# Optimization experiments

Measured on AMD Instinct MI355X. Metric: run time of the kernel, lower is better.

The kernel has to match this reference:

```python
import jax, jax.numpy as jnp
import numpy as np

B, L, D, H = 4, 2048, 1024, 64  # batch, seq, d_model, head_size

def setup_inputs() -> dict:
    key = jax.random.key(0)
    k1, k2 = jax.random.split(key)
    x = jax.random.normal(k1, (B, L, D), dtype=jnp.float32)
    # nn.Linear(d_model, head_size, bias=False) weight: [head_size, d_model]
    Wq = jax.random.normal(k2, (H, D), dtype=jnp.float32) * (1.0 / np.sqrt(D))
    return {"x": x, "Wq": Wq}

def reference(x, Wq):
    # Faithful to source bug: q, k, v ALL use the query projection.
    q = jnp.einsum('bld,hd->blh', x, Wq)
    k = q
    v = q
    d_k = x.shape[-1]  # source uses d_model, not head_size
    scores = jnp.einsum('blh,bmh->blm', q, k) / jnp.sqrt(jnp.float32(d_k))
    Lq = x.shape[1]
    causal = jnp.tril(jnp.ones((Lq, Lq), dtype=bool))
    scores = jnp.where(causal, scores, -jnp.inf)
    attn = jax.nn.softmax(scores, axis=-1)
    # dropout in eval mode -> identity
    return jnp.einsum('blm,bmh->blh', attn, v)
```

## Files before the change

### kernel.cpp

```cpp
#include <hip/hip_runtime.h>
#include <cmath>

#define Bb 4
#define Ll 2048
#define Dd 1024
#define Hh 64

#define QSCL 0.21233050f

typedef float f32x4 __attribute__((ext_vector_type(4)));
typedef short s16x8 __attribute__((ext_vector_type(8)));

__device__ __forceinline__ unsigned int cvtpk(float a, float b) {
    unsigned int r;
    asm("v_cvt_pk_bf16_f32 %0, %1, %2" : "=v"(r) : "v"(a), "v"(b));
    return r;
}

__device__ __forceinline__ void gload16(const void* g, void* l) {
    __builtin_amdgcn_global_load_lds((__attribute__((address_space(1))) const void*)g,
                                     (__attribute__((address_space(3))) void*)l, 16, 0, 0);
}

__global__ __launch_bounds__(256, 2) void proj_mfma(const float* __restrict__ x,
                                                    const float* __restrict__ Wq,
                                                    unsigned short* __restrict__ q,
                                                    unsigned short* __restrict__ qT) {
    __shared__ uint4 xs4[2][32 * 16];
    __shared__ uint4 ws4[2][32 * 64];
    const int t = threadIdx.x;
    const int lane = t & 63, w = t >> 6;
    const int m15 = lane & 15, q_ = lane >> 4;
    const int row0 = blockIdx.x * 16;
    const int kc = t & 31, rr = t >> 5;
    const float* xsrc0 = x + (size_t)(row0 + rr) * Dd + kc * 8;
    const float* xsrc1 = x + (size_t)(row0 + rr + 8) * Dd + kc * 8;

    float4 xa0 = *(const float4*)xsrc0, xb0 = *(const float4*)(xsrc0 + 4);
    float4 xa1 = *(const float4*)xsrc1, xb1 = *(const float4*)(xsrc1 + 4);
#pragma unroll
    for (int j = 0; j < 8; ++j) {
        int idx2 = t + j * 256;
        int kcw = idx2 & 31, hw = (idx2 >> 5) & 63;
        const float* wsrc = Wq + (size_t)hw * Dd + kcw * 8;
        float4 a = *(const float4*)wsrc;
        float4 b2 = *(const float4*)(wsrc + 4);
        uint4 p; p.x = cvtpk(a.x, a.y); p.y = cvtpk(a.z, a.w);
        p.z = cvtpk(b2.x, b2.y); p.w = cvtpk(b2.z, b2.w);
        ws4[0][kcw * 64 + (hw ^ kcw)] = p;
    }
    {
        uint4 p0; p0.x = cvtpk(xa0.x, xa0.y); p0.y = cvtpk(xa0.z, xa0.w);
        p0.z = cvtpk(xb0.x, xb0.y); p0.w = cvtpk(xb0.z, xb0.w);
        xs4[0][kc * 16 + (rr ^ (kc & 15))] = p0;
        uint4 p1; p1.x = cvtpk(xa1.x, xa1.y); p1.y = cvtpk(xa1.z, xa1.w);
        p1.z = cvtpk(xb1.x, xb1.y); p1.w = cvtpk(xb1.z, xb1.w);
        xs4[0][kc * 16 + ((rr + 8) ^ (kc & 15))] = p1;
    }
    xa0 = *(const float4*)(xsrc0 + 256); xb0 = *(const float4*)(xsrc0 + 260);
    xa1 = *(const float4*)(xsrc1 + 256); xb1 = *(const float4*)(xsrc1 + 260);

    f32x4 acc = {0.f, 0.f, 0.f, 0.f};
    for (int c = 0; c < 4; ++c) {
        const int p = c & 1;
        __syncthreads();
        if (c + 1 < 4) {
            const int k0n = (c + 1) * 256;
#pragma unroll
            for (int j = 0; j < 8; ++j) {
                int idx2 = t + j * 256;
                int kcw = idx2 & 31, hw = (idx2 >> 5) & 63;
                const float* wsrc = Wq + (size_t)hw * Dd + k0n + kcw * 8;
                float4 a = *(const float4*)wsrc;
                float4 b2 = *(const float4*)(wsrc + 4);
                uint4 pw; pw.x = cvtpk(a.x, a.y); pw.y = cvtpk(a.z, a.w);
                pw.z = cvtpk(b2.x, b2.y); pw.w = cvtpk(b2.z, b2.w);
                ws4[p ^ 1][kcw * 64 + (hw ^ kcw)] = pw;
            }
            uint4 p0; p0.x = cvtpk(xa0.x, xa0.y); p0.y = cvtpk(xa0.z, xa0.w);
            p0.z = cvtpk(xb0.x, xb0.y); p0.w = cvtpk(xb0.z, xb0.w);
            xs4[p ^ 1][kc * 16 + (rr ^ (kc & 15))] = p0;
            uint4 p1; p1.x = cvtpk(xa1.x, xa1.y); p1.y = cvtpk(xa1.z, xa1.w);
            p1.z = cvtpk(xb1.x, xb1.y); p1.w = cvtpk(xb1.z, xb1.w);
            xs4[p ^ 1][kc * 16 + ((rr + 8) ^ (kc & 15))] = p1;
            if (c + 2 < 4) {
                xa0 = *(const float4*)(xsrc0 + (c + 2) * 256);
                xb0 = *(const float4*)(xsrc0 + (c + 2) * 256 + 4);
                xa1 = *(const float4*)(xsrc1 + (c + 2) * 256);
                xb1 = *(const float4*)(xsrc1 + (c + 2) * 256 + 4);
            }
        }
#pragma unroll
        for (int ks = 0; ks < 8; ++ks) {
            int kk = ks * 4 + q_;
            s16x8 A = *(const s16x8*)&xs4[p][kk * 16 + (m15 ^ (kk & 15))];
            s16x8 B = *(const s16x8*)&ws4[p][kk * 64 + ((w * 16 + m15) ^ kk)];
            acc = __builtin_amdgcn_mfma_f32_16x16x32_bf16(A, B, acc, 0, 0, 0);
        }
    }
    const int h = w * 16 + m15;
    const int hc = h >> 3, he = h & 7;
    const size_t T = (size_t)(row0 >> 6);
    const int rbase = (row0 & 63) + q_ * 4;
    unsigned int a01 = cvtpk(acc[0] * QSCL, acc[1] * QSCL);
    unsigned int a23 = cvtpk(acc[2] * QSCL, acc[3] * QSCL);
    unsigned short u[4] = { (unsigned short)(a01 & 0xFFFF), (unsigned short)(a01 >> 16),
                            (unsigned short)(a23 & 0xFFFF), (unsigned short)(a23 >> 16) };
#pragma unroll
    for (int i = 0; i < 4; ++i) {
        int rsw = (rbase + i) ^ hc;
        q[((T * 8 + hc) * 64 + rsw) * 8 + he] = u[i];
    }
    unsigned int t01 = cvtpk(acc[0], acc[1]);
    unsigned int t23 = cvtpk(acc[2], acc[3]);
    const int b = row0 >> 11;
    const int m0 = (row0 & 2047) + q_ * 4;
    const int vt = m0 >> 6, cc = (m0 >> 3) & 7, me = m0 & 7;
    const int hsw = h ^ cc;
    ushort4 pk4;
    pk4.x = (unsigned short)(t01 & 0xFFFF); pk4.y = (unsigned short)(t01 >> 16);
    pk4.z = (unsigned short)(t23 & 0xFFFF); pk4.w = (unsigned short)(t23 >> 16);
    *(ushort4*)&qT[(((size_t)(b * 32 + vt) * 8 + cc) * 64 + hsw) * 8 + me] = pk4;
}

__global__ __launch_bounds__(256, 3) void flash_mfma(const unsigned short* __restrict__ qg,
                                                     const unsigned short* __restrict__ qTg,
                                                     float* __restrict__ PO,
                                                     float* __restrict__ ML) {
    const int idx = blockIdx.x;
    const int b   = blockIdx.y;
    int g = 0;
    while (2 * (g + 1) * (g + 2) <= idx) ++g;
    const int local = idx - 2 * g * (g + 1);
    const int qt = 4 * g + local / (g + 1);
    const int s  = local % (g + 1);

    __shared__ uint4 Qs4[512];
    __shared__ uint4 Ks4[2][512];
    __shared__ uint4 Vt4[2][512];
    __shared__ __align__(16) unsigned short Pb[4 * 16 * 72];
    const int t = threadIdx.x, lane = t & 63, w = t >> 6;
    const int m15 = lane & 15, q_ = lane >> 4;
    const int n_it = min(4, qt - 4 * s + 1);
    const int tb = b * 32;
    const unsigned short* qsrc = qg + (size_t)(tb + qt) * 4096;

#pragma unroll
    for (int j = 0; j < 2; ++j) {
        int off = t + j * 256;
        gload16(qsrc + (size_t)off * 8, (char*)Qs4 + off * 16);
        gload16(qg  + (size_t)(tb + s * 4) * 4096 + (size_t)off * 8, (char*)Ks4[0] + off * 16);
        gload16(qTg + (size_t)(tb + s * 4) * 4096 + (size_t)off * 8, (char*)Vt4[0] + off * 16);
    }
    f32x4 Oacc[4];
#pragma unroll
    for (int i = 0; i < 4; ++i) Oacc[i] = (f32x4){0.f, 0.f, 0.f, 0.f};
    float lr = 0.f;
    unsigned short* Pr = Pb + (w * 16 + m15) * 72;

    for (int it = 0; it < n_it; ++it) {
        const int pp = it & 1;
        __syncthreads();
        if (it + 1 < n_it) {
            const unsigned short* k2 = qg  + (size_t)(tb + s * 4 + it + 1) * 4096;
            const unsigned short* v2 = qTg + (size_t)(tb + s * 4 + it + 1) * 4096;
#pragma unroll
            for (int j = 0; j < 2; ++j) {
                int off = t + j * 256;
                gload16(k2 + (size_t)off * 8, (char*)Ks4[pp ^ 1] + off * 16);
                gload16(v2 + (size_t)off * 8, (char*)Vt4[pp ^ 1] + off * 16);
            }
        }
        f32x4 sc[4];
#pragma unroll
        for (int ct = 0; ct < 4; ++ct) sc[ct] = (f32x4){0.f, 0.f, 0.f, 0.f};
        __builtin_amdgcn_s_setprio(1);
#pragma unroll
        for (int ks = 0; ks < 2; ++ks) {
            const int hc = ks * 4 + q_;
            s16x8 Bq = *(const s16x8*)&Qs4[hc * 64 + ((w * 16 + m15) ^ hc)];
#pragma unroll
            for (int ct = 0; ct < 4; ++ct) {
                s16x8 Ak = *(const s16x8*)&Ks4[pp][hc * 64 + ((ct * 16 + m15) ^ hc)];
                sc[ct] = __builtin_amdgcn_mfma_f32_16x16x32_bf16(Ak, Bq, sc[ct], 0, 0, 0);
            }
        }
        __builtin_amdgcn_s_setprio(0);

        const bool diag = (4 * s + it) == qt;
        float v[16];
        if (diag) {
            const int rel = w * 16 + m15 - q_ * 4;
#pragma unroll
            for (int ct = 0; ct < 4; ++ct)
#pragma unroll
                for (int r = 0; r < 4; ++r)
                    v[ct * 4 + r] = (ct * 16 + r > rel) ? -INFINITY : sc[ct][r];
        } else {
#pragma unroll
            for (int ct = 0; ct < 4; ++ct)
#pragma unroll
                for (int r = 0; r < 4; ++r)
                    v[ct * 4 + r] = sc[ct][r];
        }
#pragma unroll
        for (int i = 0; i < 16; ++i) v[i] = exp2f(v[i]);
        float s01 = (v[0] + v[1]) + (v[2] + v[3]);
        float s23 = (v[4] + v[5]) + (v[6] + v[7]);
        float s45 = (v[8] + v[9]) + (v[10] + v[11]);
        float s67 = (v[12] + v[13]) + (v[14] + v[15]);
        float psum = (s01 + s23) + (s45 + s67);
        psum += __shfl_xor(psum, 16, 64);
        psum += __shfl_xor(psum, 32, 64);
        lr += psum;
#pragma unroll
        for (int ct = 0; ct < 4; ++ct) {
            uint2 pr; pr.x = cvtpk(v[ct * 4 + 0], v[ct * 4 + 1]);
            pr.y = cvtpk(v[ct * 4 + 2], v[ct * 4 + 3]);
            *(uint2*)(Pr + ct * 16 + q_ * 4) = pr;
        }
        __builtin_amdgcn_s_setprio(1);
#pragma unroll
        for (int kc2 = 0; kc2 < 2; ++kc2) {
            const int cc = kc2 * 4 + q_;
            s16x8 Bp = *(const s16x8*)(Pr + kc2 * 32 + q_ * 8);
#pragma unroll
            for (int ht = 0; ht < 4; ++ht) {
                s16x8 Av = *(const s16x8*)&Vt4[pp][cc * 64 + ((ht * 16 + m15) ^ cc)];
                Oacc[ht] = __builtin_amdgcn_mfma_f32_16x16x32_bf16(Av, Bp, Oacc[ht], 0, 0, 0);
            }
        }
        __builtin_amdgcn_s_setprio(0);
    }
    const int bq = b * 32 + qt;
    const size_t base = ((size_t)bq * 8 + s) * 4096;
#pragma unroll
    for (int ht = 0; ht < 4; ++ht)
        *(f32x4*)&PO[base + (size_t)(w * 16 + m15) * 64 + ht * 16 + q_ * 4] = Oacc[ht];
    if (q_ == 0)
        ML[((size_t)bq * 8 + s) * 64 + (w * 16 + m15)] = lr;
}

__global__ __launch_bounds__(256) void combine_k(const float* __restrict__ PO,
                                                 const float* __restrict__ ML,
                                                 float* __restrict__ out) {
    const int bq = blockIdx.x;
    const int b = bq >> 5, qt = bq & 31;
    const int ns = (qt >> 2) + 1;
    const int t = threadIdx.x;
    const int r = blockIdx.y * 32 + (t >> 3);
    const int c8 = (t & 7) * 8;
    const float* mlp = ML + (size_t)bq * 8 * 64;
    const float* pob = PO + (size_t)bq * 8 * 4096;
    float L = 0.f;
    f32x4 a0 = {0.f, 0.f, 0.f, 0.f}, a1 = a0;
    for (int si = 0; si < ns; ++si) {
        L += mlp[si * 64 + r];
        const f32x4* sp = (const f32x4*)(pob + (size_t)si * 4096 + r * 64 + c8);
        a0 += sp[0];
        a1 += sp[1];
    }
    float inv = 1.0f / L;
    f32x4* op = (f32x4*)(out + (size_t)(b * Ll + qt * 64 + r) * 64 + c8);
    op[0] = a0 * inv;
    op[1] = a1 * inv;
}

extern "C" void kernel_launch(void* const* d_in, const int* in_sizes, int n_in,
                              void* d_out, int out_size, void* d_ws, size_t ws_size,
                              hipStream_t stream) {
    const float* x  = (const float*)d_in[0];
    const float* Wq = (const float*)d_in[1];
    float* out = (float*)d_out;
    char* ws = (char*)d_ws;
    unsigned short* q   = (unsigned short*)ws;
    unsigned short* qT  = (unsigned short*)(ws + (1 << 20));
    float* PO = (float*)(ws + (2 << 20));
    float* ML = (float*)(ws + (18 << 20));

    proj_mfma<<<512, 256, 0, stream>>>(x, Wq, q, qT);
    flash_mfma<<<dim3(144, Bb), 256, 0, stream>>>(q, qT, PO, ML);
    combine_k<<<dim3(128, 2), 256, 0, stream>>>(PO, ML, out);
}
```

Measured before the change: 96.71 us.

## Process two query tiles per 512-thread flash block to share K/V loads

```diff
diff --git a/kernel.cpp b/kernel.cpp
--- a/kernel.cpp
+++ b/kernel.cpp
@@ -123,54 +123,57 @@
     *(ushort4*)&qT[(((size_t)(b * 32 + vt) * 8 + cc) * 64 + hsw) * 8 + me] = pk4;
 }
 
-__global__ __launch_bounds__(256, 3) void flash_mfma(const unsigned short* __restrict__ qg,
+__global__ __launch_bounds__(512, 4) void flash_mfma(const unsigned short* __restrict__ qg,
                                                      const unsigned short* __restrict__ qTg,
                                                      float* __restrict__ PO,
                                                      float* __restrict__ ML) {
-    const int idx = blockIdx.x;
+    const int jid = 71 - blockIdx.x;
     const int b   = blockIdx.y;
-    int g = 0;
-    while (2 * (g + 1) * (g + 2) <= idx) ++g;
-    const int local = idx - 2 * g * (g + 1);
-    const int qt = 4 * g + local / (g + 1);
-    const int s  = local % (g + 1);
-
-    __shared__ uint4 Qs4[512];
+    int G = 0;
+    while ((G + 1) * (G + 2) <= jid) ++G;
+    const int local = jid - G * (G + 1);
+    const int qp = 2 * G + local / (G + 1);
+    const int s  = local % (G + 1);
+
+    __shared__ uint4 Qs4[1024];
     __shared__ uint4 Ks4[2][512];
     __shared__ uint4 Vt4[2][512];
-    __shared__ __align__(16) unsigned short Pb[4 * 16 * 72];
+    __shared__ __align__(16) unsigned short Pb[8 * 16 * 72];
     const int t = threadIdx.x, lane = t & 63, w = t >> 6;
     const int m15 = lane & 15, q_ = lane >> 4;
-    const int n_it = min(4, qt - 4 * s + 1);
+    const int n_it = min(4, 2 * qp + 2 - 4 * s);
     const int tb = b * 32;
-    const unsigned short* qsrc = qg + (size_t)(tb + qt) * 4096;
-
+
+    const unsigned short* qsrc = qg + (size_t)(tb + 2 * qp) * 4096;
 #pragma unroll
     for (int j = 0; j < 2; ++j) {
-        int off = t + j * 256;
+        int off = t + j * 512;
         gload16(qsrc + (size_t)off * 8, (char*)Qs4 + off * 16);
-        gload16(qg  + (size_t)(tb + s * 4) * 4096 + (size_t)off * 8, (char*)Ks4[0] + off * 16);
-        gload16(qTg + (size_t)(tb + s * 4) * 4096 + (size_t)off * 8, (char*)Vt4[0] + off * 16);
-    }
+    }
+    gload16(qg  + (size_t)(tb + 4 * s) * 4096 + (size_t)t * 8, (char*)Ks4[0] + t * 16);
+    gload16(qTg + (size_t)(tb + 4 * s) * 4096 + (size_t)t * 8, (char*)Vt4[0] + t * 16);
+
     f32x4 Oacc[4];
 #pragma unroll
     for (int i = 0; i < 4; ++i) Oacc[i] = (f32x4){0.f, 0.f, 0.f, 0.f};
     float lr = 0.f;
     unsigned short* Pr = Pb + (w * 16 + m15) * 72;
+    const int qhalf = (w >> 2) * 512;
+    const int wl16  = (w & 3) * 16;
 
     for (int it = 0; it < n_it; ++it) {
         const int pp = it & 1;
+        const int kt = 4 * s + it;
         __syncthreads();
         if (it + 1 < n_it) {
-            const unsigned short* k2 = qg  + (size_t)(tb + s * 4 + it + 1) * 4096;
-            const unsigned short* v2 = qTg + (size_t)(tb + s * 4 + it + 1) * 4096;
-#pragma unroll
-            for (int j = 0; j < 2; ++j) {
-                int off = t + j * 256;
-                gload16(k2 + (size_t)off * 8, (char*)Ks4[pp ^ 1] + off * 16);
-                gload16(v2 + (size_t)off * 8, (char*)Vt4[pp ^ 1] + off * 16);
-            }
-        }
+            gload16(qg  + (size_t)(tb + kt + 1) * 4096 + (size_t)t * 8,
+                    (char*)Ks4[pp ^ 1] + t * 16);
+            gload16(qTg + (size_t)(tb + kt + 1) * 4096 + (size_t)t * 8,
+                    (char*)Vt4[pp ^ 1] + t * 16);
+        }
+        const int relw = qp * 128 + w * 16 - kt * 64;
+        if (relw + 15 < 0) continue;
+
         f32x4 sc[4];
 #pragma unroll
         for (int ct = 0; ct < 4; ++ct) sc[ct] = (f32x4){0.f, 0.f, 0.f, 0.f};
@@ -178,7 +181,7 @@
 #pragma unroll
         for (int ks = 0; ks < 2; ++ks) {
             const int hc = ks * 4 + q_;
-            s16x8 Bq = *(const s16x8*)&Qs4[hc * 64 + ((w * 16 + m15) ^ hc)];
+            s16x8 Bq = *(const s16x8*)&Qs4[qhalf + hc * 64 + ((wl16 + m15) ^ hc)];
 #pragma unroll
             for (int ct = 0; ct < 4; ++ct) {
                 s16x8 Ak = *(const s16x8*)&Ks4[pp][hc * 64 + ((ct * 16 + m15) ^ hc)];
@@ -187,10 +190,9 @@
         }
         __builtin_amdgcn_s_setprio(0);
 
-        const bool diag = (4 * s + it) == qt;
         float v[16];
-        if (diag) {
-            const int rel = w * 16 + m15 - q_ * 4;
+        if (relw < 63) {
+            const int rel = relw + m15 - q_ * 4;
 #pragma unroll
             for (int ct = 0; ct < 4; ++ct)
 #pragma unroll
@@ -232,36 +234,37 @@
         }
         __builtin_amdgcn_s_setprio(0);
     }
-    const int bq = b * 32 + qt;
-    const size_t base = ((size_t)bq * 8 + s) * 4096;
+    const int bq = b * 16 + qp;
+    const size_t base = ((size_t)bq * 8 + s) * 8192;
+    const int row = w * 16 + m15;
 #pragma unroll
     for (int ht = 0; ht < 4; ++ht)
-        *(f32x4*)&PO[base + (size_t)(w * 16 + m15) * 64 + ht * 16 + q_ * 4] = Oacc[ht];
+        *(f32x4*)&PO[base + (size_t)row * 64 + ht * 16 + q_ * 4] = Oacc[ht];
     if (q_ == 0)
-        ML[((size_t)bq * 8 + s) * 64 + (w * 16 + m15)] = lr;
+        ML[((size_t)bq * 8 + s) * 128 + row] = lr;
 }
 
 __global__ __launch_bounds__(256) void combine_k(const float* __restrict__ PO,
                                                  const float* __restrict__ ML,
                                                  float* __restrict__ out) {
     const int bq = blockIdx.x;
-    const int b = bq >> 5, qt = bq & 31;
-    const int ns = (qt >> 2) + 1;
+    const int b = bq >> 4, qp = bq & 15;
+    const int ns = (qp >> 1) + 1;
     const int t = threadIdx.x;
     const int r = blockIdx.y * 32 + (t >> 3);
     const int c8 = (t & 7) * 8;
-    const float* mlp = ML + (size_t)bq * 8 * 64;
-    const float* pob = PO + (size_t)bq * 8 * 4096;
+    const float* mlp = ML + (size_t)bq * 8 * 128;
+    const float* pob = PO + (size_t)bq * 8 * 8192;
     float L = 0.f;
     f32x4 a0 = {0.f, 0.f, 0.f, 0.f}, a1 = a0;
     for (int si = 0; si < ns; ++si) {
-        L += mlp[si * 64 + r];
-        const f32x4* sp = (const f32x4*)(pob + (size_t)si * 4096 + r * 64 + c8);
+        L += mlp[si * 128 + r];
+        const f32x4* sp = (const f32x4*)(pob + (size_t)si * 8192 + r * 64 + c8);
         a0 += sp[0];
         a1 += sp[1];
     }
     float inv = 1.0f / L;
-    f32x4* op = (f32x4*)(out + (size_t)(b * Ll + qt * 64 + r) * 64 + c8);
+    f32x4* op = (f32x4*)(out + (size_t)(b * Ll + qp * 128 + r) * 64 + c8);
     op[0] = a0 * inv;
     op[1] = a1 * inv;
 }
@@ -279,6 +282,6 @@
     float* ML = (float*)(ws + (18 << 20));
 
     proj_mfma<<<512, 256, 0, stream>>>(x, Wq, q, qT);
-    flash_mfma<<<dim3(144, Bb), 256, 0, stream>>>(q, qT, PO, ML);
-    combine_k<<<dim3(128, 2), 256, 0, stream>>>(PO, ML, out);
-}
+    flash_mfma<<<dim3(72, Bb), 512, 0, stream>>>(q, qT, PO, ML);
+    combine_k<<<dim3(64, 4), 256, 0, stream>>>(PO, ML, out);
+}
```

Result: no change. 97.24 us (+0.5%).
